# Kernel tuning notes

Hardware: AMD Instinct MI355X
Metric: run time of the kernel (lower is better)

Reference implementation:

```python
import jax, jax.numpy as jnp
import numpy as np

D_MODEL = 1024
N_HEADS = 16
D_HEAD = D_MODEL // N_HEADS
EPS = 1e-6


def setup_inputs() -> dict:
    key = jax.random.key(0)
    ks = jax.random.split(key, 11)
    N, L, S = 4, 4096, 4096
    scale = 1.0 / np.sqrt(D_MODEL)
    inp = {
        "queries": jax.random.normal(ks[0], (N, L, D_MODEL), jnp.float32),
        "keys": jax.random.normal(ks[1], (N, S, D_MODEL), jnp.float32),
        "values": jax.random.normal(ks[2], (N, S, D_MODEL), jnp.float32),
        "Wq": jax.random.normal(ks[3], (D_MODEL, D_MODEL), jnp.float32) * scale,
        "bq": jnp.zeros((D_MODEL,), jnp.float32),
        "Wk": jax.random.normal(ks[4], (D_MODEL, D_MODEL), jnp.float32) * scale,
        "bk": jnp.zeros((D_MODEL,), jnp.float32),
        "Wv": jax.random.normal(ks[5], (D_MODEL, D_MODEL), jnp.float32) * scale,
        "bv": jnp.zeros((D_MODEL,), jnp.float32),
        "Wo": jax.random.normal(ks[6], (D_MODEL, D_MODEL), jnp.float32) * scale,
        "bo": jnp.zeros((D_MODEL,), jnp.float32),
    }
    return inp


def reference(queries, keys, values, Wq, bq, Wk, bk, Wv, bv, Wo, bo):
    N, L, _ = queries.shape
    S = keys.shape[1]
    H, Dh = N_HEADS, D_HEAD
    # projections (torch Linear: x @ W.T + b)
    q = (queries @ Wq.T + bq).reshape(N, L, H, Dh)
    k = (keys @ Wk.T + bk).reshape(N, S, H, Dh)
    v = (values @ Wv.T + bv).reshape(N, S, H, Dh)
    # elu+1 feature map
    Q = jax.nn.elu(q) + 1.0
    K = jax.nn.elu(k) + 1.0
    # KV summary: [N,H,Dv,Dh]
    KV = jnp.einsum('nshd,nshm->nhmd', K, v)
    # normalizer: [N,L,H]
    Z = 1.0 / (jnp.einsum('nlhd,nhd->nlh', Q, K.sum(axis=1)) + EPS)
    # output per head: [N,L,H,Dv]
    V = jnp.einsum('nlhd,nhmd,nlh->nlhm', Q, KV, Z)
    out = V.reshape(N, L, H * Dh) @ Wo.T + bo
    return out
```

## Files before the change

### kernel.cpp

```cpp
#include <hip/hip_runtime.h>
#include <hip/hip_bf16.h>

typedef __attribute__((ext_vector_type(8))) short short8;
typedef __attribute__((ext_vector_type(4))) short short4v;
typedef __attribute__((ext_vector_type(4))) float f32x4;

#define MFMA16(a, b, c) __builtin_amdgcn_mfma_f32_16x16x32_bf16(a, b, c, 0, 0, 0)

__device__ __forceinline__ unsigned short f2bf(float f) {
    unsigned int u = __float_as_uint(f);
    unsigned int r = u + 0x7fffu + ((u >> 16) & 1u);
    return (unsigned short)(r >> 16);
}
__device__ __forceinline__ float bf2f(unsigned short h) {
    return __uint_as_float(((unsigned int)h) << 16);
}
__device__ __forceinline__ unsigned int pk2(float lo, float hi) {
    return (unsigned int)f2bf(lo) | ((unsigned int)f2bf(hi) << 16);
}

__device__ __forceinline__ void async16(const void* g, void* l) {
    __builtin_amdgcn_global_load_lds(
        (const __attribute__((address_space(1))) unsigned int*)g,
        (__attribute__((address_space(3))) unsigned int*)l, 16, 0, 0);
}

#define S_BARRIER() asm volatile("s_barrier" ::: "memory")
#define SCHED_FENCE() __builtin_amdgcn_sched_barrier(0)

__global__ __launch_bounds__(256) void cvt_all(const float* __restrict__ q,
                                               const float* __restrict__ k,
                                               const float* __restrict__ v,
                                               const float* __restrict__ Wq,
                                               const float* __restrict__ Wk,
                                               const float* __restrict__ Wv,
                                               const float* __restrict__ Wo,
                                               unsigned short* __restrict__ qb,
                                               unsigned short* __restrict__ kb,
                                               unsigned short* __restrict__ vb,
                                               unsigned short* __restrict__ Wqb,
                                               unsigned short* __restrict__ Wkb,
                                               unsigned short* __restrict__ Wvb,
                                               unsigned short* __restrict__ Wob) {
    int b = blockIdx.x;
    const float* in;
    unsigned short* out;
    int lb, nb, n8;
    if (b < 6144) {
        int s = b >> 11;
        lb = b & 2047; nb = 2048; n8 = 2097152;
        in = s == 0 ? q : s == 1 ? k : v;
        out = s == 0 ? qb : s == 1 ? kb : vb;
    } else {
        int s = b - 6144;
        int w = s >> 7;
        lb = s & 127; nb = 128; n8 = 131072;
        in = w == 0 ? Wq : w == 1 ? Wk : w == 2 ? Wv : Wo;
        out = w == 0 ? Wqb : w == 1 ? Wkb : w == 2 ? Wvb : Wob;
    }
    for (int i = lb * 256 + threadIdx.x; i < n8; i += nb * 256) {
        float4 v0 = reinterpret_cast<const float4*>(in)[2 * i];
        float4 v1 = reinterpret_cast<const float4*>(in)[2 * i + 1];
        uint4 p;
        p.x = pk2(v0.x, v0.y); p.y = pk2(v0.z, v0.w);
        p.z = pk2(v1.x, v1.y); p.w = pk2(v1.z, v1.w);
        reinterpret_cast<uint4*>(out)[i] = p;
    }
}

__device__ __forceinline__ void gemm_body(const unsigned short* __restrict__ A,
                                          const unsigned short* __restrict__ B,
                                          const float* __restrict__ bias,
                                          void* __restrict__ out,
                                          int mode, char* lds, int bid) {
    const int tid = threadIdx.x;
    const int lane = tid & 63, wid = tid >> 6;
    const int wr = wid >> 2, wc = wid & 3;
    const int lr = lane & 15, lg = lane >> 4;

    const int swz = (bid & 7) * 32 + (bid >> 3);
    const int bm = swz >> 2, bn = swz & 3;
    const long row0 = (long)bm * 256;
    const long col0 = (long)bn * 256;

    const unsigned short* srcA[2];
    const unsigned short* srcB[2];
    int dstOff[2];
#pragma unroll
    for (int g = 0; g < 2; ++g) {
        int s = g * 512 + tid;
        int pr = s >> 3;
        int dc = (s & 7) ^ (pr & 7);
        srcA[g] = A + (row0 + (pr & 63) + 128 * (pr >> 6)) * 1024 + dc * 8;
        srcB[g] = B + (col0 + pr) * 1024 + dc * 8;
        dstOff[g] = s * 16;
    }

#define STG_AQ(BB, Q, KT) do {                                                  \
        async16(srcA[0] + (Q) * 65536 + (KT) * 64,                              \
                lds + (BB) * 65536 + (Q) * 16384 + dstOff[0]);                  \
        async16(srcA[1] + (Q) * 65536 + (KT) * 64,                              \
                lds + (BB) * 65536 + (Q) * 16384 + dstOff[1]); } while (0)
#define STG_BH(BB, H, KT) do {                                                  \
        async16(srcB[0] + (H) * 131072 + (KT) * 64,                             \
                lds + (BB) * 65536 + 32768 + (H) * 16384 + dstOff[0]);          \
        async16(srcB[1] + (H) * 131072 + (KT) * 64,                             \
                lds + (BB) * 65536 + 32768 + (H) * 16384 + dstOff[1]); } while (0)

    const int ch0 = (((0 * 4 + lg) ^ (lr & 7)) << 4);
    const int ch1 = (((1 * 4 + lg) ^ (lr & 7)) << 4);
    const int aB0 = (64 * wr + lr) * 128 + ch0;
    const int aB1 = (64 * wr + lr) * 128 + ch1;
    const int bB0 = 32768 + (wc >> 1) * 16384 + ((wc & 1) * 64 + lr) * 128 + ch0;
    const int bB1 = 32768 + (wc >> 1) * 16384 + ((wc & 1) * 64 + lr) * 128 + ch1;

    f32x4 acc[8][4] = {};
    short8 b0[4], b1[4];

#define GATE4() do { asm volatile("s_waitcnt vmcnt(4)" ::: "memory"); SCHED_FENCE(); } while (0)
#define GATE0() do { asm volatile("s_waitcnt vmcnt(0)" ::: "memory"); SCHED_FENCE(); } while (0)
#define MFMA_BLOCK(MB, BV) do {                                                 \
        S_BARRIER();                                                            \
        asm volatile("s_waitcnt lgkmcnt(0)" ::: "memory");                      \
        SCHED_FENCE();                                                          \
        __builtin_amdgcn_s_setprio(1);                                          \
        _Pragma("unroll") for (int m = 0; m < 4; ++m)                           \
            _Pragma("unroll") for (int n = 0; n < 4; ++n)                       \
                acc[(MB) + m][n] = MFMA16(a[m], BV[n], acc[(MB) + m][n]);       \
        __builtin_amdgcn_s_setprio(0);                                          \
        SCHED_FENCE();                                                          \
        S_BARRIER(); } while (0)
#define LOAD_A(BUFB, ABASE, Q) do {                                             \
        _Pragma("unroll") for (int m = 0; m < 4; ++m)                           \
            a[m] = *(const short8*)(lds + (BUFB) + (Q) * 16384 + (ABASE) + m * 2048); } while (0)
#define LOAD_B(BUFB, BBASE, BV) do {                                            \
        _Pragma("unroll") for (int n = 0; n < 4; ++n)                           \
            BV[n] = *(const short8*)(lds + (BUFB) + (BBASE) + n * 2048); } while (0)

    STG_AQ(0, 0, 0); STG_BH(0, 0, 0); STG_BH(0, 1, 0); STG_AQ(0, 1, 0);
    STG_AQ(1, 0, 1); STG_BH(1, 0, 1);
    GATE4();
    S_BARRIER();

#pragma unroll 1
    for (int t = 0; t < 7; ++t) {
        const int ktA = 2 * t + 1, ktB = 2 * t + 2, ktC = 2 * t + 3;
        { short8 a[4]; LOAD_B(0, bB0, b0); LOAD_A(0, aB0, 0); STG_BH(1, 1, ktA); MFMA_BLOCK(0, b0); }
        { short8 a[4]; LOAD_B(0, bB1, b1); LOAD_A(0, aB1, 0); STG_AQ(1, 1, ktA); MFMA_BLOCK(0, b1); }
        { short8 a[4]; LOAD_A(0, aB0, 1); STG_AQ(0, 0, ktB); MFMA_BLOCK(4, b0); }
        { short8 a[4]; LOAD_A(0, aB1, 1); STG_BH(0, 0, ktB); GATE4(); MFMA_BLOCK(4, b1); }
        { short8 a[4]; LOAD_B(65536, bB0, b0); LOAD_A(65536, aB0, 0); STG_BH(0, 1, ktB); MFMA_BLOCK(0, b0); }
        { short8 a[4]; LOAD_B(65536, bB1, b1); LOAD_A(65536, aB1, 0); STG_AQ(0, 1, ktB); MFMA_BLOCK(0, b1); }
        { short8 a[4]; LOAD_A(65536, aB0, 1); STG_AQ(1, 0, ktC); MFMA_BLOCK(4, b0); }
        { short8 a[4]; LOAD_A(65536, aB1, 1); STG_BH(1, 0, ktC); GATE4(); MFMA_BLOCK(4, b1); }
    }
    {
        { short8 a[4]; LOAD_B(0, bB0, b0); LOAD_A(0, aB0, 0); STG_BH(1, 1, 15); MFMA_BLOCK(0, b0); }
        { short8 a[4]; LOAD_B(0, bB1, b1); LOAD_A(0, aB1, 0); STG_AQ(1, 1, 15); MFMA_BLOCK(0, b1); }
        { short8 a[4]; LOAD_A(0, aB0, 1); MFMA_BLOCK(4, b0); }
        { short8 a[4]; LOAD_A(0, aB1, 1); GATE0(); MFMA_BLOCK(4, b1); }
        { short8 a[4]; LOAD_B(65536, bB0, b0); LOAD_A(65536, aB0, 0); MFMA_BLOCK(0, b0); }
        { short8 a[4]; LOAD_B(65536, bB1, b1); LOAD_A(65536, aB1, 0); MFMA_BLOCK(0, b1); }
        { short8 a[4]; LOAD_A(65536, aB0, 1); MFMA_BLOCK(4, b0); }
        { short8 a[4]; LOAD_A(65536, aB1, 1); MFMA_BLOCK(4, b1); }
    }
#undef STG_AQ
#undef STG_BH
#undef GATE4
#undef GATE0
#undef MFMA_BLOCK
#undef LOAD_A
#undef LOAD_B

    const int r4 = lg * 4;
    if (mode == 0 || mode == 3) {
        char* ep = lds + wid * 4608;
#pragma unroll
        for (int m = 0; m < 8; ++m) {
#pragma unroll
            for (int n = 0; n < 4; ++n) {
                float bcol = bias[col0 + wc * 64 + n * 16 + lr];
#pragma unroll
                for (int j = 0; j < 4; ++j) {
                    float v = acc[m][n][j] + bcol;
                    if (mode == 0) v = v > 0.f ? v + 1.f : __expf(v);
                    *(float*)(ep + (((lg * 4 + j) * 68) + n * 16 + lr) * 4) = v;
                }
            }
            asm volatile("s_waitcnt lgkmcnt(0)" ::: "memory");
            SCHED_FENCE();
            long R0b = row0 + wr * 128 + m * 16;
            if (mode == 0) {
                unsigned short* O = (unsigned short*)out;
#pragma unroll
                for (int i = 0; i < 2; ++i) {
                    int r = i * 8 + (lane >> 3), c8 = (lane & 7) * 8;
                    float4 u0 = *(const float4*)(ep + (r * 68 + c8) * 4);
                    float4 u1 = *(const float4*)(ep + (r * 68 + c8 + 4) * 4);
                    uint4 w;
                    w.x = pk2(u0.x, u0.y); w.y = pk2(u0.z, u0.w);
                    w.z = pk2(u1.x, u1.y); w.w = pk2(u1.z, u1.w);
                    *(uint4*)(O + (R0b + r) * 1024 + col0 + wc * 64 + c8) = w;
                }
            } else {
                float* O = (float*)out;
#pragma unroll
                for (int i = 0; i < 4; ++i) {
                    int r = i * 4 + (lane >> 4), c4 = (lane & 15) * 4;
                    float4 u = *(const float4*)(ep + (r * 68 + c4) * 4);
                    *(float4*)(O + (R0b + r) * 1024 + col0 + wc * 64 + c4) = u;
                }
            }
            asm volatile("s_waitcnt lgkmcnt(0)" ::: "memory");
            SCHED_FENCE();
        }
    } else {
#pragma unroll
        for (int m = 0; m < 8; ++m) {
#pragma unroll
            for (int n = 0; n < 4; ++n) {
                long col = col0 + wc * 64 + n * 16 + lr;
                float bcol = bias[col];
                long R0 = row0 + wr * 128 + m * 16 + r4;
                unsigned short* O = (unsigned short*)out;
                long nb = R0 >> 12;
                long s = R0 & 4095;
                short4v pack;
#pragma unroll
                for (int j = 0; j < 4; ++j) {
                    float v = acc[m][n][j] + bcol;
                    if (mode == 1) v = v > 0.f ? v + 1.f : __expf(v);
                    pack[j] = (short)f2bf(v);
                }
                *(short4v*)(O + ((nb << 10) + col) * 4096 + s) = pack;
            }
        }
    }
}

__global__ __launch_bounds__(512, 1) void proj_gemm(const unsigned short* __restrict__ qb,
                                                    const unsigned short* __restrict__ kb,
                                                    const unsigned short* __restrict__ vb,
                                                    const unsigned short* __restrict__ Wqb,
                                                    const unsigned short* __restrict__ Wkb,
                                                    const unsigned short* __restrict__ Wvb,
                                                    const float* __restrict__ bq,
                                                    const float* __restrict__ bk,
                                                    const float* __restrict__ bv,
                                                    unsigned short* __restrict__ Qm,
                                                    unsigned short* __restrict__ Kt,
                                                    unsigned short* __restrict__ vT) {
    __shared__ __align__(16) char lds[131072];
    int seg = blockIdx.x >> 8;
    int bid = blockIdx.x & 255;
    const unsigned short* A = seg == 0 ? qb : seg == 1 ? kb : vb;
    const unsigned short* B = seg == 0 ? Wqb : seg == 1 ? Wkb : Wvb;
    const float* bias = seg == 0 ? bq : seg == 1 ? bk : bv;
    void* out = seg == 0 ? (void*)Qm : seg == 1 ? (void*)Kt : (void*)vT;
    gemm_body(A, B, bias, out, seg, lds, bid);
}

__global__ __launch_bounds__(512, 1) void out_gemm(const unsigned short* __restrict__ Vbuf,
                                                   const unsigned short* __restrict__ Wob,
                                                   const float* __restrict__ bo,
                                                   float* __restrict__ out) {
    __shared__ __align__(16) char lds[131072];
    gemm_body(Vbuf, Wob, bo, out, 3, lds, blockIdx.x);
}

__global__ __launch_bounds__(256) void kv_kernel(const unsigned short* __restrict__ Kt,
                                                 const unsigned short* __restrict__ vT,
                                                 float* __restrict__ KV,
                                                 float* __restrict__ Ksum) {
    int b = blockIdx.x;
    int sc = b & 7, h = (b >> 3) & 15, n = b >> 7;
    const int tid = threadIdx.x, lane = tid & 63, wave = tid >> 6;
    long base = ((long)(n * 1024 + h * 64)) * 4096 + sc * 512;
    const unsigned short* Kp = Kt + base;
    const unsigned short* Vp = vT + base;
    const int lr = lane & 15, lk = (lane >> 4) * 8;

    f32x4 acc[4] = {};
    float ksa[4] = {0.f, 0.f, 0.f, 0.f};
    for (int s0 = 0; s0 < 512; s0 += 32) {
        short8 a = *(const short8*)(Vp + (long)(wave * 16 + lr) * 4096 + s0 + lk);
#pragma unroll
        for (int d4 = 0; d4 < 4; ++d4) {
            short8 bb = *(const short8*)(Kp + (long)(d4 * 16 + lr) * 4096 + s0 + lk);
            acc[d4] = MFMA16(a, bb, acc[d4]);
            if (wave == 0) {
                float t = 0.f;
#pragma unroll
                for (int e = 0; e < 8; ++e) t += bf2f((unsigned short)bb[e]);
                ksa[d4] += t;
            }
        }
    }
    float* KVb = KV + (long)(n * 16 + h) * 4096;
#pragma unroll
    for (int d4 = 0; d4 < 4; ++d4)
#pragma unroll
        for (int j = 0; j < 4; ++j) {
            int m = wave * 16 + (lane >> 4) * 4 + j;
            int d = d4 * 16 + lr;
            atomicAdd(KVb + m * 64 + d, acc[d4][j]);
        }
    if (wave == 0) {
#pragma unroll
        for (int d4 = 0; d4 < 4; ++d4) {
            float t = ksa[d4];
            t += __shfl_xor(t, 16, 64);
            t += __shfl_xor(t, 32, 64);
            if (lane < 16) atomicAdd(Ksum + n * 1024 + h * 64 + d4 * 16 + lane, t);
        }
    }
}

__global__ __launch_bounds__(256) void attn_kernel(const unsigned short* __restrict__ Qm,
                                                   const float* __restrict__ KV,
                                                   const float* __restrict__ Ksum,
                                                   unsigned short* __restrict__ Vbuf) {
    __shared__ unsigned short Qs[128 * 64];
    __shared__ unsigned short KVs[64 * 64];
    __shared__ float zin[128];
    __shared__ float ks[64];
    int b = blockIdx.x;
    int lc = b & 31, h = (b >> 5) & 15, n = b >> 9;
    int tid = threadIdx.x, lane = tid & 63, wave = tid >> 6;
    long l0 = (long)n * 4096 + lc * 128;

    const unsigned short* Qg = Qm + (l0 + (tid >> 3)) * 1024 + h * 64 + (tid & 7) * 8;
    char* QsB = (char*)Qs + (wave << 10);
#pragma unroll
    for (int it = 0; it < 4; ++it)
        async16(Qg + (long)it * 32 * 1024, QsB + it * 4096);

    const float* kvp = KV + (long)(n * 16 + h) * 4096;
    for (int i = tid * 4; i < 4096; i += 1024) {
        float4 v = *reinterpret_cast<const float4*>(kvp + i);
        short4v p;
        p[0] = (short)f2bf(v.x); p[1] = (short)f2bf(v.y);
        p[2] = (short)f2bf(v.z); p[3] = (short)f2bf(v.w);
        *(short4v*)(KVs + i) = p;
    }
    if (tid < 64) ks[tid] = Ksum[n * 1024 + h * 64 + tid];
    __syncthreads();

    {
        int row = tid >> 1, half = tid & 1;
        float den = 0.f;
        const unsigned short* qrow = Qs + row * 64 + half * 32;
#pragma unroll
        for (int d = 0; d < 32; ++d) den += bf2f(qrow[d]) * ks[half * 32 + d];
        den += __shfl_xor(den, 1, 64);
        if (half == 0) zin[row] = 1.0f / (den + 1e-6f);
    }
    __syncthreads();

    const int lr = lane & 15, lk = (lane >> 4) * 8;
    f32x4 acc[2][4] = {};
#pragma unroll
    for (int kk = 0; kk < 2; ++kk) {
        short8 a0 = *(const short8*)(Qs + (wave * 32 + lr) * 64 + kk * 32 + lk);
        short8 a1 = *(const short8*)(Qs + (wave * 32 + 16 + lr) * 64 + kk * 32 + lk);
#pragma unroll
        for (int nn = 0; nn < 4; ++nn) {
            short8 bb = *(const short8*)(KVs + (nn * 16 + lr) * 64 + kk * 32 + lk);
            acc[0][nn] = MFMA16(a0, bb, acc[0][nn]);
            acc[1][nn] = MFMA16(a1, bb, acc[1][nn]);
        }
    }

    {
        char* ep = (char*)Qs + wave * 4096;
#pragma unroll
        for (int mi = 0; mi < 2; ++mi) {
#pragma unroll
            for (int nn = 0; nn < 4; ++nn)
#pragma unroll
                for (int j = 0; j < 4; ++j) {
                    int rloc = (lane >> 4) * 4 + j;
                    float v = acc[mi][nn][j] * zin[wave * 32 + mi * 16 + rloc];
                    *(float*)(ep + (rloc * 64 + nn * 16 + lr) * 4) = v;
                }
            asm volatile("s_waitcnt lgkmcnt(0)" ::: "memory");
            SCHED_FENCE();
#pragma unroll
            for (int i = 0; i < 2; ++i) {
                int r = i * 8 + (lane >> 3), c8 = (lane & 7) * 8;
                float4 u0 = *(const float4*)(ep + (r * 64 + c8) * 4);
                float4 u1 = *(const float4*)(ep + (r * 64 + c8 + 4) * 4);
                uint4 w;
                w.x = pk2(u0.x, u0.y); w.y = pk2(u0.z, u0.w);
                w.z = pk2(u1.x, u1.y); w.w = pk2(u1.z, u1.w);
                *(uint4*)(Vbuf + (l0 + wave * 32 + mi * 16 + r) * 1024 + h * 64 + c8) = w;
            }
            asm volatile("s_waitcnt lgkmcnt(0)" ::: "memory");
            SCHED_FENCE();
        }
    }
}

extern "C" void kernel_launch(void* const* d_in, const int* in_sizes, int n_in,
                              void* d_out, int out_size, void* d_ws, size_t ws_size,
                              hipStream_t stream) {
    const float* queries = (const float*)d_in[0];
    const float* keys    = (const float*)d_in[1];
    const float* values  = (const float*)d_in[2];
    const float* Wq = (const float*)d_in[3];
    const float* bq = (const float*)d_in[4];
    const float* Wk = (const float*)d_in[5];
    const float* bk = (const float*)d_in[6];
    const float* Wv = (const float*)d_in[7];
    const float* bv = (const float*)d_in[8];
    const float* Wo = (const float*)d_in[9];
    const float* bo = (const float*)d_in[10];
    float* out = (float*)d_out;

    char* ws = (char*)d_ws;
    const size_t SZ = (size_t)16384 * 1024 * 2;
    const size_t WSZ = (size_t)1024 * 1024 * 2;
    unsigned short* qb  = (unsigned short*)(ws);
    unsigned short* kb  = (unsigned short*)(ws + SZ);
    unsigned short* vb  = (unsigned short*)(ws + 2 * SZ);
    unsigned short* Wqb = (unsigned short*)(ws + 3 * SZ);
    unsigned short* Wkb = (unsigned short*)(ws + 3 * SZ + WSZ);
    unsigned short* Wvb = (unsigned short*)(ws + 3 * SZ + 2 * WSZ);
    unsigned short* Wob = (unsigned short*)(ws + 3 * SZ + 3 * WSZ);
    unsigned short* Qm  = (unsigned short*)(ws + 3 * SZ + 4 * WSZ);
    unsigned short* Kt  = (unsigned short*)(ws + 4 * SZ + 4 * WSZ);
    unsigned short* vT  = (unsigned short*)(ws + 5 * SZ + 4 * WSZ);
    float* KVf = (float*)(ws + 6 * SZ + 4 * WSZ);
    float* Ksf = (float*)(ws + 6 * SZ + 4 * WSZ + 1048576);
    unsigned short* Vbuf = qb;

    hipMemsetAsync(KVf, 0, 1048576 + 16384, stream);

    cvt_all<<<6656, 256, 0, stream>>>(queries, keys, values, Wq, Wk, Wv, Wo,
                                      qb, kb, vb, Wqb, Wkb, Wvb, Wob);

    proj_gemm<<<768, 512, 0, stream>>>(qb, kb, vb, Wqb, Wkb, Wvb, bq, bk, bv, Qm, Kt, vT);

    kv_kernel<<<512, 256, 0, stream>>>(Kt, vT, KVf, Ksf);
    attn_kernel<<<2048, 256, 0, stream>>>(Qm, KVf, Ksf, Vbuf);

    out_gemm<<<256, 512, 0, stream>>>(Vbuf, Wob, bo, out);
}
```

Measured before the change: 255.7 us.

## Fuse fp32-to-bf16 activation conversion into projection GEMM A-operand loads

The standalone conversion pass over the large q/k/v activations is removed. The projection GEMM now streams fp32 activations directly into LDS through a new triple-buffered pipeline and converts them to bf16 in registers with v_cvt_pk_bf16_f32 before the MFMAs. Only the weights are still pre-converted, by a smaller kernel. This saves writing and re-reading roughly 100MB of bf16 intermediates, at the cost of double the A-operand bytes through LDS, extra conversion ALU work in the inner loop, and a larger LDS footprint.

```diff
diff --git a/kernel.cpp b/kernel.cpp
--- a/kernel.cpp
+++ b/kernel.cpp
@@ -18,6 +18,11 @@
 __device__ __forceinline__ unsigned int pk2(float lo, float hi) {
     return (unsigned int)f2bf(lo) | ((unsigned int)f2bf(hi) << 16);
 }
+__device__ __forceinline__ unsigned int cvtpk(float lo, float hi) {
+    unsigned int r;
+    asm("v_cvt_pk_bf16_f32 %0, %1, %2" : "=v"(r) : "v"(lo), "v"(hi));
+    return r;
+}
 
 __device__ __forceinline__ void async16(const void* g, void* l) {
     __builtin_amdgcn_global_load_lds(
@@ -28,37 +33,19 @@
 #define S_BARRIER() asm volatile("s_barrier" ::: "memory")
 #define SCHED_FENCE() __builtin_amdgcn_sched_barrier(0)
 
-__global__ __launch_bounds__(256) void cvt_all(const float* __restrict__ q,
-                                               const float* __restrict__ k,
-                                               const float* __restrict__ v,
-                                               const float* __restrict__ Wq,
-                                               const float* __restrict__ Wk,
-                                               const float* __restrict__ Wv,
-                                               const float* __restrict__ Wo,
-                                               unsigned short* __restrict__ qb,
-                                               unsigned short* __restrict__ kb,
-                                               unsigned short* __restrict__ vb,
-                                               unsigned short* __restrict__ Wqb,
-                                               unsigned short* __restrict__ Wkb,
-                                               unsigned short* __restrict__ Wvb,
-                                               unsigned short* __restrict__ Wob) {
-    int b = blockIdx.x;
-    const float* in;
-    unsigned short* out;
-    int lb, nb, n8;
-    if (b < 6144) {
-        int s = b >> 11;
-        lb = b & 2047; nb = 2048; n8 = 2097152;
-        in = s == 0 ? q : s == 1 ? k : v;
-        out = s == 0 ? qb : s == 1 ? kb : vb;
-    } else {
-        int s = b - 6144;
-        int w = s >> 7;
-        lb = s & 127; nb = 128; n8 = 131072;
-        in = w == 0 ? Wq : w == 1 ? Wk : w == 2 ? Wv : Wo;
-        out = w == 0 ? Wqb : w == 1 ? Wkb : w == 2 ? Wvb : Wob;
-    }
-    for (int i = lb * 256 + threadIdx.x; i < n8; i += nb * 256) {
+__global__ __launch_bounds__(256) void cvt4_kernel(const float* __restrict__ w0,
+                                                   const float* __restrict__ w1,
+                                                   const float* __restrict__ w2,
+                                                   const float* __restrict__ w3,
+                                                   unsigned short* __restrict__ o0,
+                                                   unsigned short* __restrict__ o1,
+                                                   unsigned short* __restrict__ o2,
+                                                   unsigned short* __restrict__ o3) {
+    int wsel = blockIdx.x >> 7;
+    int lb = blockIdx.x & 127;
+    const float* in = wsel == 0 ? w0 : wsel == 1 ? w1 : wsel == 2 ? w2 : w3;
+    unsigned short* out = wsel == 0 ? o0 : wsel == 1 ? o1 : wsel == 2 ? o2 : o3;
+    for (int i = lb * 256 + threadIdx.x; i < 131072; i += 32768) {
         float4 v0 = reinterpret_cast<const float4*>(in)[2 * i];
         float4 v1 = reinterpret_cast<const float4*>(in)[2 * i + 1];
         uint4 p;
@@ -68,11 +55,209 @@
     }
 }
 
-__device__ __forceinline__ void gemm_body(const unsigned short* __restrict__ A,
+__device__ __forceinline__ void gemm_f32a(const float* __restrict__ A,
                                           const unsigned short* __restrict__ B,
                                           const float* __restrict__ bias,
                                           void* __restrict__ out,
                                           int mode, char* lds, int bid) {
+    const int tid = threadIdx.x;
+    const int lane = tid & 63, wid = tid >> 6;
+    const int wr = wid >> 2, wc = wid & 3;
+    const int lr = lane & 15, lg = lane >> 4;
+
+    const int swz = (bid & 7) * 32 + (bid >> 3);
+    const int bm = swz >> 2, bn = swz & 3;
+    const long row0 = (long)bm * 256;
+    const long col0 = (long)bn * 256;
+
+    const float* srcA[4];
+#pragma unroll
+    for (int g = 0; g < 4; ++g) {
+        int s = g * 512 + tid;
+        int pr = s >> 3;
+        int dc = (s & 7) ^ (pr & 7);
+        srcA[g] = A + (row0 + pr) * 1024 + dc * 4;
+    }
+    const unsigned short* srcB[2];
+#pragma unroll
+    for (int g = 0; g < 2; ++g) {
+        int s = g * 512 + tid;
+        int pr = s >> 3;
+        int dc = (s & 7) ^ (pr & 7);
+        srcB[g] = B + (col0 + pr + 128 * (dc >> 2)) * 1024 + (dc & 3) * 8;
+    }
+    const int dst = tid * 16;
+
+#define STAGE_A(BUF, KT) do {                                                   \
+        async16(srcA[0] + (KT) * 32, (BUF) + dst);                              \
+        async16(srcA[1] + (KT) * 32, (BUF) + 8192 + dst);                       \
+        async16(srcA[2] + (KT) * 32, (BUF) + 16384 + dst);                      \
+        async16(srcA[3] + (KT) * 32, (BUF) + 24576 + dst); } while (0)
+#define STAGE_B(BUF, KT) do {                                                   \
+        async16(srcB[0] + (KT) * 32, (BUF) + 32768 + dst);                      \
+        async16(srcB[1] + (KT) * 32, (BUF) + 40960 + dst); } while (0)
+
+    int offA[8];
+#pragma unroll
+    for (int m = 0; m < 8; ++m)
+        offA[m] = (wr * 128 + m * 16 + lr) * 128 + (((2 * lg) ^ (lr & 7)) << 4);
+    int offB[4];
+#pragma unroll
+    for (int n = 0; n < 4; ++n)
+        offB[n] = 32768 + ((wc & 1) * 64 + n * 16 + lr) * 128 +
+                  ((((wc >> 1) * 4 + lg) ^ (lr & 7)) << 4);
+
+    f32x4 acc[8][4] = {};
+
+    char* p0 = lds;
+    char* p1 = lds + 49152;
+    char* p2 = lds + 98304;
+
+    STAGE_A(p0, 0); STAGE_B(p0, 0);
+    STAGE_A(p1, 1); STAGE_B(p1, 1);
+    asm volatile("s_waitcnt vmcnt(6)" ::: "memory");
+    SCHED_FENCE();
+    S_BARRIER();
+
+#pragma unroll 1
+    for (int kt = 0; kt < 32; ++kt) {
+        short8 b[4];
+        {
+            float4 a0[4], a1[4];
+#pragma unroll
+            for (int m = 0; m < 4; ++m) {
+                a0[m] = *(const float4*)(p0 + offA[m]);
+                a1[m] = *(const float4*)(p0 + (offA[m] ^ 16));
+            }
+#pragma unroll
+            for (int n = 0; n < 4; ++n) b[n] = *(const short8*)(p0 + offB[n]);
+            SCHED_FENCE();
+            if (kt < 30) STAGE_A(p2, kt + 2);
+            asm volatile("s_waitcnt lgkmcnt(0)" ::: "memory");
+            SCHED_FENCE();
+            short8 af[4];
+#pragma unroll
+            for (int m = 0; m < 4; ++m) {
+                union { unsigned int u[4]; short8 s; } cv;
+                cv.u[0] = cvtpk(a0[m].x, a0[m].y);
+                cv.u[1] = cvtpk(a0[m].z, a0[m].w);
+                cv.u[2] = cvtpk(a1[m].x, a1[m].y);
+                cv.u[3] = cvtpk(a1[m].z, a1[m].w);
+                af[m] = cv.s;
+            }
+            __builtin_amdgcn_s_setprio(1);
+#pragma unroll
+            for (int m = 0; m < 4; ++m)
+#pragma unroll
+                for (int n = 0; n < 4; ++n)
+                    acc[m][n] = MFMA16(af[m], b[n], acc[m][n]);
+            __builtin_amdgcn_s_setprio(0);
+            SCHED_FENCE();
+            S_BARRIER();
+        }
+        {
+            float4 a0[4], a1[4];
+#pragma unroll
+            for (int m = 0; m < 4; ++m) {
+                a0[m] = *(const float4*)(p0 + offA[4 + m]);
+                a1[m] = *(const float4*)(p0 + (offA[4 + m] ^ 16));
+            }
+            SCHED_FENCE();
+            if (kt < 30) STAGE_B(p2, kt + 2);
+            if (kt < 30) {
+                asm volatile("s_waitcnt vmcnt(6)" ::: "memory");
+            } else {
+                asm volatile("s_waitcnt vmcnt(0)" ::: "memory");
+            }
+            SCHED_FENCE();
+            asm volatile("s_waitcnt lgkmcnt(0)" ::: "memory");
+            SCHED_FENCE();
+            short8 af[4];
+#pragma unroll
+            for (int m = 0; m < 4; ++m) {
+                union { unsigned int u[4]; short8 s; } cv;
+                cv.u[0] = cvtpk(a0[m].x, a0[m].y);
+                cv.u[1] = cvtpk(a0[m].z, a0[m].w);
+                cv.u[2] = cvtpk(a1[m].x, a1[m].y);
+                cv.u[3] = cvtpk(a1[m].z, a1[m].w);
+                af[m] = cv.s;
+            }
+            __builtin_amdgcn_s_setprio(1);
+#pragma unroll
+            for (int m = 0; m < 4; ++m)
+#pragma unroll
+                for (int n = 0; n < 4; ++n)
+                    acc[4 + m][n] = MFMA16(af[m], b[n], acc[4 + m][n]);
+            __builtin_amdgcn_s_setprio(0);
+            SCHED_FENCE();
+            S_BARRIER();
+        }
+        char* t_ = p0; p0 = p1; p1 = p2; p2 = t_;
+    }
+#undef STAGE_A
+#undef STAGE_B
+
+    const int r4 = lg * 4;
+    if (mode == 0) {
+        char* ep = lds + wid * 4608;
+#pragma unroll
+        for (int m = 0; m < 8; ++m) {
+#pragma unroll
+            for (int n = 0; n < 4; ++n) {
+                float bcol = bias[col0 + wc * 64 + n * 16 + lr];
+#pragma unroll
+                for (int j = 0; j < 4; ++j) {
+                    float v = acc[m][n][j] + bcol;
+                    v = v > 0.f ? v + 1.f : __expf(v);
+                    *(float*)(ep + (((lg * 4 + j) * 68) + n * 16 + lr) * 4) = v;
+                }
+            }
+            asm volatile("s_waitcnt lgkmcnt(0)" ::: "memory");
+            SCHED_FENCE();
+            long R0b = row0 + wr * 128 + m * 16;
+            unsigned short* O = (unsigned short*)out;
+#pragma unroll
+            for (int i = 0; i < 2; ++i) {
+                int r = i * 8 + (lane >> 3), c8 = (lane & 7) * 8;
+                float4 u0 = *(const float4*)(ep + (r * 68 + c8) * 4);
+                float4 u1 = *(const float4*)(ep + (r * 68 + c8 + 4) * 4);
+                uint4 w;
+                w.x = pk2(u0.x, u0.y); w.y = pk2(u0.z, u0.w);
+                w.z = pk2(u1.x, u1.y); w.w = pk2(u1.z, u1.w);
+                *(uint4*)(O + (R0b + r) * 1024 + col0 + wc * 64 + c8) = w;
+            }
+            asm volatile("s_waitcnt lgkmcnt(0)" ::: "memory");
+            SCHED_FENCE();
+        }
+    } else {
+#pragma unroll
+        for (int m = 0; m < 8; ++m) {
+#pragma unroll
+            for (int n = 0; n < 4; ++n) {
+                long col = col0 + wc * 64 + n * 16 + lr;
+                float bcol = bias[col];
+                long R0 = row0 + wr * 128 + m * 16 + r4;
+                unsigned short* O = (unsigned short*)out;
+                long nb = R0 >> 12;
+                long s = R0 & 4095;
+                short4v pack;
+#pragma unroll
+                for (int j = 0; j < 4; ++j) {
+                    float v = acc[m][n][j] + bcol;
+                    if (mode == 1) v = v > 0.f ? v + 1.f : __expf(v);
+                    pack[j] = (short)f2bf(v);
+                }
+                *(short4v*)(O + ((nb << 10) + col) * 4096 + s) = pack;
+            }
+        }
+    }
+}
+
+__device__ __forceinline__ void gemm_body(const unsigned short* __restrict__ A,
+                                          const unsigned short* __restrict__ B,
+                                          const float* __restrict__ bias,
+                                          float* __restrict__ out,
+                                          char* lds, int bid) {
     const int tid = threadIdx.x;
     const int lane = tid & 63, wid = tid >> 6;
     const int wr = wid >> 2, wc = wid & 3;
@@ -107,8 +292,8 @@
         async16(srcB[1] + (H) * 131072 + (KT) * 64,                             \
                 lds + (BB) * 65536 + 32768 + (H) * 16384 + dstOff[1]); } while (0)
 
-    const int ch0 = (((0 * 4 + lg) ^ (lr & 7)) << 4);
-    const int ch1 = (((1 * 4 + lg) ^ (lr & 7)) << 4);
+    const int ch0 = ((lg ^ (lr & 7)) << 4);
+    const int ch1 = (((4 + lg) ^ (lr & 7)) << 4);
     const int aB0 = (64 * wr + lr) * 128 + ch0;
     const int aB1 = (64 * wr + lr) * 128 + ch1;
     const int bB0 = 32768 + (wc >> 1) * 16384 + ((wc & 1) * 64 + lr) * 128 + ch0;
@@ -172,8 +357,7 @@
 #undef LOAD_A
 #undef LOAD_B
 
-    const int r4 = lg * 4;
-    if (mode == 0 || mode == 3) {
+    {
         char* ep = lds + wid * 4608;
 #pragma unroll
         for (int m = 0; m < 8; ++m) {
@@ -181,66 +365,27 @@
             for (int n = 0; n < 4; ++n) {
                 float bcol = bias[col0 + wc * 64 + n * 16 + lr];
 #pragma unroll
-                for (int j = 0; j < 4; ++j) {
-                    float v = acc[m][n][j] + bcol;
-                    if (mode == 0) v = v > 0.f ? v + 1.f : __expf(v);
-                    *(float*)(ep + (((lg * 4 + j) * 68) + n * 16 + lr) * 4) = v;
-                }
+                for (int j = 0; j < 4; ++j)
+                    *(float*)(ep + (((lg * 4 + j) * 68) + n * 16 + lr) * 4) = acc[m][n][j] + bcol;
             }
             asm volatile("s_waitcnt lgkmcnt(0)" ::: "memory");
             SCHED_FENCE();
             long R0b = row0 + wr * 128 + m * 16;
-            if (mode == 0) {
-                unsigned short* O = (unsigned short*)out;
-#pragma unroll
-                for (int i = 0; i < 2; ++i) {
-                    int r = i * 8 + (lane >> 3), c8 = (lane & 7) * 8;
-                    float4 u0 = *(const float4*)(ep + (r * 68 + c8) * 4);
-                    float4 u1 = *(const float4*)(ep + (r * 68 + c8 + 4) * 4);
-                    uint4 w;
-                    w.x = pk2(u0.x, u0.y); w.y = pk2(u0.z, u0.w);
-                    w.z = pk2(u1.x, u1.y); w.w = pk2(u1.z, u1.w);
-                    *(uint4*)(O + (R0b + r) * 1024 + col0 + wc * 64 + c8) = w;
-                }
-            } else {
-                float* O = (float*)out;
-#pragma unroll
-                for (int i = 0; i < 4; ++i) {
-                    int r = i * 4 + (lane >> 4), c4 = (lane & 15) * 4;
-                    float4 u = *(const float4*)(ep + (r * 68 + c4) * 4);
-                    *(float4*)(O + (R0b + r) * 1024 + col0 + wc * 64 + c4) = u;
-                }
-            }
-            asm volatile("s_waitcnt lgkmcnt(0)" ::: "memory");
-            SCHED_FENCE();
-        }
-    } else {
-#pragma unroll
-        for (int m = 0; m < 8; ++m) {
-#pragma unroll
-            for (int n = 0; n < 4; ++n) {
-                long col = col0 + wc * 64 + n * 16 + lr;
-                float bcol = bias[col];
-                long R0 = row0 + wr * 128 + m * 16 + r4;
-                unsigned short* O = (unsigned short*)out;
-                long nb = R0 >> 12;
-                long s = R0 & 4095;
-                short4v pack;
-#pragma unroll
-                for (int j = 0; j < 4; ++j) {
-                    float v = acc[m][n][j] + bcol;
-                    if (mode == 1) v = v > 0.f ? v + 1.f : __expf(v);
-                    pack[j] = (short)f2bf(v);
-                }
-                *(short4v*)(O + ((nb << 10) + col) * 4096 + s) = pack;
-            }
-        }
-    }
-}
-
-__global__ __launch_bounds__(512, 1) void proj_gemm(const unsigned short* __restrict__ qb,
-                                                    const unsigned short* __restrict__ kb,
-                                                    const unsigned short* __restrict__ vb,
+#pragma unroll
+            for (int i = 0; i < 4; ++i) {
+                int r = i * 4 + (lane >> 4), c4 = (lane & 15) * 4;
+                float4 u = *(const float4*)(ep + (r * 68 + c4) * 4);
+                *(float4*)(out + (R0b + r) * 1024 + col0 + wc * 64 + c4) = u;
+            }
+            asm volatile("s_waitcnt lgkmcnt(0)" ::: "memory");
+            SCHED_FENCE();
+        }
+    }
+}
+
+__global__ __launch_bounds__(512, 1) void proj_gemm(const float* __restrict__ q,
+                                                    const float* __restrict__ k,
+                                                    const float* __restrict__ v,
                                                     const unsigned short* __restrict__ Wqb,
                                                     const unsigned short* __restrict__ Wkb,
                                                     const unsigned short* __restrict__ Wvb,
@@ -250,14 +395,14 @@
                                                     unsigned short* __restrict__ Qm,
                                                     unsigned short* __restrict__ Kt,
                                                     unsigned short* __restrict__ vT) {
-    __shared__ __align__(16) char lds[131072];
+    __shared__ __align__(16) char lds[147456];
     int seg = blockIdx.x >> 8;
     int bid = blockIdx.x & 255;
-    const unsigned short* A = seg == 0 ? qb : seg == 1 ? kb : vb;
+    const float* A = seg == 0 ? q : seg == 1 ? k : v;
     const unsigned short* B = seg == 0 ? Wqb : seg == 1 ? Wkb : Wvb;
     const float* bias = seg == 0 ? bq : seg == 1 ? bk : bv;
     void* out = seg == 0 ? (void*)Qm : seg == 1 ? (void*)Kt : (void*)vT;
-    gemm_body(A, B, bias, out, seg, lds, bid);
+    gemm_f32a(A, B, bias, out, seg, lds, bid);
 }
 
 __global__ __launch_bounds__(512, 1) void out_gemm(const unsigned short* __restrict__ Vbuf,
@@ -265,7 +410,7 @@
                                                    const float* __restrict__ bo,
                                                    float* __restrict__ out) {
     __shared__ __align__(16) char lds[131072];
-    gemm_body(Vbuf, Wob, bo, out, 3, lds, blockIdx.x);
+    gemm_body(Vbuf, Wob, bo, out, lds, blockIdx.x);
 }
 
 __global__ __launch_bounds__(256) void kv_kernel(const unsigned short* __restrict__ Kt,
@@ -420,26 +565,23 @@
     char* ws = (char*)d_ws;
     const size_t SZ = (size_t)16384 * 1024 * 2;
     const size_t WSZ = (size_t)1024 * 1024 * 2;
-    unsigned short* qb  = (unsigned short*)(ws);
-    unsigned short* kb  = (unsigned short*)(ws + SZ);
-    unsigned short* vb  = (unsigned short*)(ws + 2 * SZ);
-    unsigned short* Wqb = (unsigned short*)(ws + 3 * SZ);
-    unsigned short* Wkb = (unsigned short*)(ws + 3 * SZ + WSZ);
-    unsigned short* Wvb = (unsigned short*)(ws + 3 * SZ + 2 * WSZ);
-    unsigned short* Wob = (unsigned short*)(ws + 3 * SZ + 3 * WSZ);
-    unsigned short* Qm  = (unsigned short*)(ws + 3 * SZ + 4 * WSZ);
-    unsigned short* Kt  = (unsigned short*)(ws + 4 * SZ + 4 * WSZ);
-    unsigned short* vT  = (unsigned short*)(ws + 5 * SZ + 4 * WSZ);
-    float* KVf = (float*)(ws + 6 * SZ + 4 * WSZ);
-    float* Ksf = (float*)(ws + 6 * SZ + 4 * WSZ + 1048576);
-    unsigned short* Vbuf = qb;
+    unsigned short* Wqb = (unsigned short*)(ws);
+    unsigned short* Wkb = (unsigned short*)(ws + WSZ);
+    unsigned short* Wvb = (unsigned short*)(ws + 2 * WSZ);
+    unsigned short* Wob = (unsigned short*)(ws + 3 * WSZ);
+    unsigned short* Qm   = (unsigned short*)(ws + 4 * WSZ);
+    unsigned short* Kt   = (unsigned short*)(ws + 4 * WSZ + SZ);
+    unsigned short* vT   = (unsigned short*)(ws + 4 * WSZ + 2 * SZ);
+    unsigned short* Vbuf = (unsigned short*)(ws + 4 * WSZ + 3 * SZ);
+    float* KVf = (float*)(ws + 4 * WSZ + 4 * SZ);
+    float* Ksf = (float*)(ws + 4 * WSZ + 4 * SZ + 1048576);
 
     hipMemsetAsync(KVf, 0, 1048576 + 16384, stream);
 
-    cvt_all<<<6656, 256, 0, stream>>>(queries, keys, values, Wq, Wk, Wv, Wo,
-                                      qb, kb, vb, Wqb, Wkb, Wvb, Wob);
-
-    proj_gemm<<<768, 512, 0, stream>>>(qb, kb, vb, Wqb, Wkb, Wvb, bq, bk, bv, Qm, Kt, vT);
+    cvt4_kernel<<<512, 256, 0, stream>>>(Wq, Wk, Wv, Wo, Wqb, Wkb, Wvb, Wob);
+
+    proj_gemm<<<768, 512, 0, stream>>>(queries, keys, values, Wqb, Wkb, Wvb,
+                                       bq, bk, bv, Qm, Kt, vT);
 
     kv_kernel<<<512, 256, 0, stream>>>(Kt, vT, KVf, Ksf);
     attn_kernel<<<2048, 256, 0, stream>>>(Qm, KVf, Ksf, Vbuf);
```

Result: faster. 233.3 us, median of 3 (-8.7%).
